# Kernel optimization log

Hardware: AMD Instinct MI355X
Metric: run time of the kernel (lower is better)

The kernel has to match this reference:

```python
import jax, jax.numpy as jnp
import numpy as np

N_PAPER = 100000
N_LABEL = 128
E_CITES = 1600000
E_IS = 100000
F_IN = 128
HID = 128
EMB = 64


def _seg_sum(data, ids, n):
    return jax.ops.segment_sum(data, ids, num_segments=n)


def gcn_conv(x, src, dst, W, b, n):
    # PyG GCNConv: out = D^-1/2 (A+I) D^-1/2 (x W) + b
    h = x @ W
    deg = _seg_sum(jnp.ones(src.shape[0], h.dtype), dst, n) + 1.0  # +1 self loop
    dinv = jax.lax.rsqrt(deg)
    norm = dinv[src] * dinv[dst]                      # [E]
    out = _seg_sum(h[src] * norm[:, None], dst, n)    # neighbor messages
    out = out + (dinv * dinv)[:, None] * h            # self-loop term
    return out + b


def graph_conv(x_src, x_dst, src, dst, W_rel, b_rel, W_root, n_dst):
    # PyG GraphConv: out = lin_rel(sum_j x_j) + lin_root(x_i)
    agg = _seg_sum(x_src[src], dst, n_dst)
    return agg @ W_rel + b_rel + x_dst @ W_root


def hetero_layer(xp, xl, cs, cd, iss, isd, p):
    # outputs onto 'paper' from cites (GCN) and rev_is (GraphConv label->paper): mean of 2
    o_cites = gcn_conv(xp, cs, cd, p['gcn_W'], p['gcn_b'], N_PAPER)
    o_rev = graph_conv(xl, xp, isd, iss, p['rev_relW'], p['rev_relb'], p['rev_rootW'], N_PAPER)
    o_paper = 0.5 * (o_cites + o_rev)
    # output onto 'label' from is (GraphConv paper->label): single conv, mean is identity
    o_label = graph_conv(xp, xl, iss, isd, p['is_relW'], p['is_relb'], p['is_rootW'], N_LABEL)
    return o_paper, o_label


def _init_params(key, d_in, d_out, pfx):
    ks = jax.random.split(key, 8)
    s = 1.0 / np.sqrt(d_in)
    return {
        'gcn_W': jax.random.normal(ks[0], (d_in, d_out), jnp.float32) * s,
        'gcn_b': jnp.zeros((d_out,), jnp.float32),
        'is_relW': jax.random.normal(ks[1], (d_in, d_out), jnp.float32) * s,
        'is_relb': jnp.zeros((d_out,), jnp.float32),
        'is_rootW': jax.random.normal(ks[2], (d_in, d_out), jnp.float32) * s,
        'rev_relW': jax.random.normal(ks[3], (d_in, d_out), jnp.float32) * s,
        'rev_relb': jnp.zeros((d_out,), jnp.float32),
        'rev_rootW': jax.random.normal(ks[4], (d_in, d_out), jnp.float32) * s,
    }


def setup_inputs() -> dict:
    key = jax.random.key(0)
    ks = jax.random.split(key, 10)
    inp = {
        'x_paper': jax.random.normal(ks[0], (N_PAPER, F_IN), jnp.float32),
        'x_label': jax.random.normal(ks[1], (N_LABEL, F_IN), jnp.float32),
        'cites_src': jax.random.randint(ks[2], (E_CITES,), 0, N_PAPER, jnp.int32),
        'cites_dst': jax.random.randint(ks[3], (E_CITES,), 0, N_PAPER, jnp.int32),
        'is_src': jax.random.randint(ks[4], (E_IS,), 0, N_PAPER, jnp.int32),
        'is_dst': jax.random.randint(ks[5], (E_IS,), 0, N_LABEL, jnp.int32),
    }
    p1 = _init_params(ks[6], F_IN, HID, 'l1')
    p2 = _init_params(ks[7], HID, EMB, 'l2')
    for k, v in p1.items():
        inp['l1_' + k] = v
    for k, v in p2.items():
        inp['l2_' + k] = v
    return inp


def reference(x_paper, x_label, cites_src, cites_dst, is_src, is_dst,
              l1_gcn_W, l1_gcn_b, l1_is_relW, l1_is_relb, l1_is_rootW,
              l1_rev_relW, l1_rev_relb, l1_rev_rootW,
              l2_gcn_W, l2_gcn_b, l2_is_relW, l2_is_relb, l2_is_rootW,
              l2_rev_relW, l2_rev_relb, l2_rev_rootW):
    p1 = dict(gcn_W=l1_gcn_W, gcn_b=l1_gcn_b, is_relW=l1_is_relW, is_relb=l1_is_relb,
              is_rootW=l1_is_rootW, rev_relW=l1_rev_relW, rev_relb=l1_rev_relb, rev_rootW=l1_rev_rootW)
    p2 = dict(gcn_W=l2_gcn_W, gcn_b=l2_gcn_b, is_relW=l2_is_relW, is_relb=l2_is_relb,
              is_rootW=l2_is_rootW, rev_relW=l2_rev_relW, rev_relb=l2_rev_relb, rev_rootW=l2_rev_rootW)
    hp, hl = hetero_layer(x_paper, x_label, cites_src, cites_dst, is_src, is_dst, p1)
    hp, hl = jax.nn.relu(hp), jax.nn.relu(hl)
    zp, zl = hetero_layer(hp, hl, cites_src, cites_dst, is_src, is_dst, p2)
    return zp, zl
```

## Files before the change

### kernel.cpp

```cpp
#include <hip/hip_runtime.h>
#include <hip/hip_bf16.h>

#define N_PAPER 100000
#define N_LABEL 128
#define E_CITES 1600000
#define E_IS    100000
#define NBKT    98
#define A2_CHUNK 2048
#define LSPLIT  8
#define CAPC    24576
#define CAPR    2048
#define CAPL    8192

typedef __bf16 bf16x8 __attribute__((ext_vector_type(8)));
typedef float  f32x4  __attribute__((ext_vector_type(4)));
typedef float  f32x2  __attribute__((ext_vector_type(2)));

static __device__ __forceinline__ float bf_lo(unsigned u) {
    union { unsigned u; float f; } v; v.u = u << 16; return v.f;
}
static __device__ __forceinline__ float bf_hi(unsigned u) {
    union { unsigned u; float f; } v; v.u = u & 0xffff0000u; return v.f;
}
static __device__ __forceinline__ unsigned pk_bf(float a, float b) {
    __hip_bfloat16 x = __float2bfloat16(a), y = __float2bfloat16(b);
    unsigned short ux = *(unsigned short*)&x, uy = *(unsigned short*)&y;
    return (unsigned)ux | ((unsigned)uy << 16);
}
static __device__ __forceinline__ unsigned char enc_fp8(float v) {
    return (unsigned char)(__builtin_amdgcn_cvt_pk_fp8_f32(v, v, 0, false) & 0xFF);
}
static __device__ __forceinline__ void dec4(unsigned u, float* o) {
    f32x2 a = __builtin_amdgcn_cvt_pk_f32_fp8((int)u, false);
    f32x2 b = __builtin_amdgcn_cvt_pk_f32_fp8((int)u, true);
    o[0] = a[0]; o[1] = a[1]; o[2] = b[0]; o[3] = b[1];
}

#define NSC ((E_CITES + A2_CHUNK - 1) / A2_CHUNK)
#define NSI ((E_IS + A2_CHUNK - 1) / A2_CHUNK)
__global__ __launch_bounds__(256) void fused_scatter(
    const int* __restrict__ cd, const int* __restrict__ cs,
    const int* __restrict__ iss, const int* __restrict__ isd,
    int* __restrict__ bcur_c, unsigned* __restrict__ ebuf_c,
    int* __restrict__ bcur_r, unsigned* __restrict__ ebuf_r,
    int* __restrict__ bcur_l, unsigned* __restrict__ ebuf_l)
{
    __shared__ int sk[A2_CHUNK], sv[A2_CHUNK];
    __shared__ int h[128], base[128], cur[128];
    int b = blockIdx.x, t = threadIdx.x;
    const int* key; const int* val; int E, shift, b0, cap; int* bcur; unsigned* ebuf;
    if (b < NSC)            { key = cd;  val = cs;  E = E_CITES; bcur = bcur_c; ebuf = ebuf_c; shift = 10; cap = CAPC; b0 = b; }
    else if (b < NSC + NSI) { key = iss; val = isd; E = E_IS;    bcur = bcur_r; ebuf = ebuf_r; shift = 10; cap = CAPR; b0 = b - NSC; }
    else                    { key = isd; val = iss; E = E_IS;    bcur = bcur_l; ebuf = ebuf_l; shift = 0;  cap = CAPL; b0 = b - NSC - NSI; }
    int e0 = b0 * A2_CHUNK;
    int n = min(A2_CHUNK, E - e0);
    for (int i = t; i < 128; i += 256) h[i] = 0;
    __syncthreads();
    for (int i = t; i < n; i += 256) {
        int k = key[e0 + i], v = val[e0 + i];
        sk[i] = k; sv[i] = v;
        atomicAdd(&h[k >> shift], 1);
    }
    __syncthreads();
    for (int i = t; i < 128; i += 256) { base[i] = atomicAdd(&bcur[i], h[i]); cur[i] = 0; }
    __syncthreads();
    for (int i = t; i < n; i += 256) {
        int bb = sk[i] >> shift;
        int p = base[bb] + atomicAdd(&cur[bb], 1);
        ebuf[(size_t)bb * cap + p] = ((unsigned)(sk[i] & 1023) << 17) | (unsigned)sv[i];
    }
}

__global__ __launch_bounds__(1024) void fused_csr(
    const unsigned* __restrict__ ebuf_c, const int* __restrict__ bcnt_c,
    int2* __restrict__ rp2_c, int* __restrict__ col_c, float* __restrict__ dinv,
    const unsigned* __restrict__ ebuf_r, const int* __restrict__ bcnt_r,
    int2* __restrict__ rp2_r, int* __restrict__ col_r)
{
    __shared__ int hist[1024];
    __shared__ int sc[1024];
    int bb = blockIdx.x, t = threadIdx.x;
    const unsigned* ebuf; const int* bcnt; int2* rp2; int* col; float* dv; int b, cap;
    if (bb < NBKT) { ebuf = ebuf_c; bcnt = bcnt_c; rp2 = rp2_c; col = col_c; dv = dinv; b = bb; cap = CAPC; }
    else           { ebuf = ebuf_r; bcnt = bcnt_r; rp2 = rp2_r; col = col_r; dv = nullptr; b = bb - NBKT; cap = CAPR; }
    size_t s = (size_t)b * cap;
    int n = bcnt[b];
    hist[t] = 0;
    __syncthreads();
    for (int i = t; i < n; i += 1024)
        atomicAdd(&hist[ebuf[s + i] >> 17], 1);
    __syncthreads();
    int v = hist[t];
    sc[t] = v;
    __syncthreads();
    for (int off = 1; off < 1024; off <<= 1) {
        int u = (t >= off) ? sc[t - off] : 0;
        __syncthreads();
        sc[t] += u;
        __syncthreads();
    }
    int excl = sc[t] - v;
    int node = b * 1024 + t;
    if (node < N_PAPER) {
        rp2[node] = make_int2((int)(s + excl), (int)(s + excl + v));
        if (dv) dv[node] = rsqrtf((float)v + 1.0f);
    }
    __syncthreads();
    hist[t] = (int)(s + excl);
    __syncthreads();
    for (int i = t; i < n; i += 1024) {
        unsigned u = ebuf[s + i];
        int p = atomicAdd(&hist[u >> 17], 1);
        col[p] = (int)(u & 0x1FFFFu);
    }
}

__global__ __launch_bounds__(256) void fused_prep(
    const float* __restrict__ g1, const float* __restrict__ r1, __hip_bfloat16* __restrict__ Wp1,
    const float* __restrict__ g2, const float* __restrict__ r2, __hip_bfloat16* __restrict__ Wp2,
    const float* __restrict__ xl, const float* __restrict__ W1rev, float* __restrict__ yrev1)
{
    int b = blockIdx.x, t = threadIdx.x;
    if (b < 128 + 64) {
        bool big = (b < 128);
        const float* g = big ? g1 : g2;
        const float* r = big ? r1 : r2;
        __hip_bfloat16* Wp = big ? Wp1 : Wp2;
        int DG = big ? 128 : 64;
        int i = (big ? b : (b - 128)) * 256 + t;
        int j    = i & 7;
        int lane = (i >> 3) & 63;
        int ks   = (i >> 9) & 3;
        int nt   = i >> 11;
        int k = ks * 32 + (lane >> 4) * 8 + j;
        int c = nt * 16 + (lane & 15);
        float v = (c < DG) ? g[k * DG + c] : r[k * DG + (c - DG)];
        Wp[i] = __float2bfloat16(v);
        return;
    }
    __shared__ float xrow[2][128];
    int bb = b - (128 + 64);
    int half = t >> 7, tt = t & 127;
    int l = bb * 2 + half;
    xrow[half][tt] = xl[(size_t)l * 128 + tt];
    __syncthreads();
    float o = 0.f;
    for (int k = 0; k < 128; ++k) o = fmaf(xrow[half][k], W1rev[k * 128 + tt], o);
    yrev1[(size_t)l * 128 + tt] = o;
}

template<int DG, bool AF32>
__global__ __launch_bounds__(512) void gemm_mfma(
    const void* __restrict__ Av, const __hip_bfloat16* __restrict__ Wp,
    const float* __restrict__ dinv,
    unsigned char* __restrict__ Hg, __hip_bfloat16* __restrict__ Hr, int M)
{
    constexpr int NT2 = 2 * DG / 16;
    __shared__ __hip_bfloat16 wlds[NT2 * 2048];
    int tid = threadIdx.x;
    for (int i = tid; i < NT2 * 256; i += 512)
        *(bf16x8*)(wlds + (size_t)i * 8) = *(const bf16x8*)(Wp + (size_t)i * 8);
    __syncthreads();

    int wv = tid >> 6, lane = tid & 63;
    int m0 = blockIdx.x * 128 + wv * 16;
    int row = m0 + (lane & 15);
    int rowc = min(row, M - 1);
    int kg = lane >> 4;

    bf16x8 a[4];
    if constexpr (AF32) {
        const float* ap = (const float*)Av + (size_t)rowc * 128 + kg * 8;
        #pragma unroll
        for (int ks = 0; ks < 4; ++ks) {
            float4 v0 = *(const float4*)(ap + ks * 32);
            float4 v1 = *(const float4*)(ap + ks * 32 + 4);
            bf16x8 f;
            f[0] = (__bf16)v0.x; f[1] = (__bf16)v0.y; f[2] = (__bf16)v0.z; f[3] = (__bf16)v0.w;
            f[4] = (__bf16)v1.x; f[5] = (__bf16)v1.y; f[6] = (__bf16)v1.z; f[7] = (__bf16)v1.w;
            a[ks] = f;
        }
    } else {
        const __hip_bfloat16* ap = (const __hip_bfloat16*)Av + (size_t)rowc * 128 + kg * 8;
        #pragma unroll
        for (int ks = 0; ks < 4; ++ks)
            a[ks] = *(const bf16x8*)(ap + ks * 32);
    }

    f32x4 acc[NT2] = {};
    #pragma unroll
    for (int ks = 0; ks < 4; ++ks) {
        #pragma unroll
        for (int nt = 0; nt < NT2; ++nt) {
            bf16x8 b = *(const bf16x8*)(wlds + ((size_t)(nt * 4 + ks) * 64 + lane) * 8);
            acc[nt] = __builtin_amdgcn_mfma_f32_16x16x32_bf16(a[ks], b, acc[nt], 0, 0, 0);
        }
    }

    int rbase = m0 + (lane >> 4) * 4;
    int c = lane & 15;
    float ds[4];
    #pragma unroll
    for (int r = 0; r < 4; ++r) {
        int rr = rbase + r;
        ds[r] = (rr < M) ? dinv[rr] : 1.f;
    }
    #pragma unroll
    for (int nt = 0; nt < NT2; ++nt) {
        bool isG = (nt < DG / 16);
        if (isG) {
            int cc = nt * 16 + c;
            #pragma unroll
            for (int r = 0; r < 4; ++r) {
                int rr = rbase + r;
                if (rr < M) Hg[(size_t)rr * DG + cc] = enc_fp8(acc[nt][r] * ds[r]);
            }
        } else {
            int cc = (nt - DG / 16) * 16 + c;
            #pragma unroll
            for (int r = 0; r < 4; ++r) {
                int rr = rbase + r;
                if (rr < M) Hr[(size_t)rr * DG + cc] = __float2bfloat16(acc[nt][r]);
            }
        }
    }
}

template<int D, bool RELU, typename OutT>
__global__ __launch_bounds__(256) void paper_assemble(
    const unsigned char* __restrict__ Hg, const __hip_bfloat16* __restrict__ Hr,
    const int2* __restrict__ rp2_c, const int* __restrict__ col_c,
    const float* __restrict__ dinv,
    const int2* __restrict__ rp2_r, const int* __restrict__ col_r,
    const float* __restrict__ yrev,
    const float* __restrict__ gcn_b, const float* __restrict__ rev_relb,
    OutT* __restrict__ out)
{
    constexpr int GL = (D == 128) ? 16 : 8;
    constexpr int NGRP = 64 / GL;
    int w = (int)((blockIdx.x * 256 + threadIdx.x) >> 6);
    if (w >= N_PAPER) return;
    int lane = threadIdx.x & 63;
    int grp = lane / GL, sub = lane % GL;
    unsigned d0 = (unsigned)sub * 8;
    f32x2 a2[4] = {};
    int2 se = rp2_c[w];
    int e = se.y;
    int j = se.x + grp;
    for (; j + NGRP < e; j += 2 * NGRP) {
        unsigned o0 = (unsigned)col_c[j] * D + d0;
        unsigned o1 = (unsigned)col_c[j + NGRP] * D + d0;
        uint2 u = *(const uint2*)(Hg + o0);
        uint2 v = *(const uint2*)(Hg + o1);
        a2[0] += __builtin_amdgcn_cvt_pk_f32_fp8((int)u.x, false);
        a2[1] += __builtin_amdgcn_cvt_pk_f32_fp8((int)u.x, true);
        a2[2] += __builtin_amdgcn_cvt_pk_f32_fp8((int)u.y, false);
        a2[3] += __builtin_amdgcn_cvt_pk_f32_fp8((int)u.y, true);
        a2[0] += __builtin_amdgcn_cvt_pk_f32_fp8((int)v.x, false);
        a2[1] += __builtin_amdgcn_cvt_pk_f32_fp8((int)v.x, true);
        a2[2] += __builtin_amdgcn_cvt_pk_f32_fp8((int)v.y, false);
        a2[3] += __builtin_amdgcn_cvt_pk_f32_fp8((int)v.y, true);
    }
    if (j < e) {
        unsigned o0 = (unsigned)col_c[j] * D + d0;
        uint2 u = *(const uint2*)(Hg + o0);
        a2[0] += __builtin_amdgcn_cvt_pk_f32_fp8((int)u.x, false);
        a2[1] += __builtin_amdgcn_cvt_pk_f32_fp8((int)u.x, true);
        a2[2] += __builtin_amdgcn_cvt_pk_f32_fp8((int)u.y, false);
        a2[3] += __builtin_amdgcn_cvt_pk_f32_fp8((int)u.y, true);
    }
    float acc[8];
    #pragma unroll
    for (int k = 0; k < 8; ++k) acc[k] = a2[k >> 1][k & 1];
    #pragma unroll
    for (int k = 0; k < 8; ++k) {
        #pragma unroll
        for (int off = GL; off < 64; off <<= 1)
            acc[k] += __shfl_xor(acc[k], off);
    }
    if (grp != 0) return;

    float di = dinv[w];
    float res[8], sg[8], sr[8];
    const unsigned char* hg = Hg + ((unsigned)w * D + d0);
    const __hip_bfloat16* hr = Hr + (size_t)w * D + d0;
    uint2 ug = *(const uint2*)hg;
    dec4(ug.x, sg); dec4(ug.y, sg + 4);
    uint4 ur = *(const uint4*)hr;
    sr[0] = bf_lo(ur.x); sr[1] = bf_hi(ur.x); sr[2] = bf_lo(ur.y); sr[3] = bf_hi(ur.y);
    sr[4] = bf_lo(ur.z); sr[5] = bf_hi(ur.z); sr[6] = bf_lo(ur.w); sr[7] = bf_hi(ur.w);
    #pragma unroll
    for (int k = 0; k < 8; ++k)
        res[k] = di * (acc[k] + sg[k]) + sr[k] + gcn_b[d0 + k] + rev_relb[d0 + k];

    int2 se2 = rp2_r[w];
    for (int jj = se2.x; jj < se2.y; ++jj) {
        const float* yr = yrev + (size_t)col_r[jj] * D + d0;
        #pragma unroll
        for (int k = 0; k < 8; ++k) res[k] += yr[k];
    }
    #pragma unroll
    for (int k = 0; k < 8; ++k) {
        res[k] *= 0.5f;
        if (RELU) res[k] = fmaxf(res[k], 0.f);
    }
    if constexpr (sizeof(OutT) == 2) {
        uint4 o = make_uint4(pk_bf(res[0], res[1]), pk_bf(res[2], res[3]),
                             pk_bf(res[4], res[5]), pk_bf(res[6], res[7]));
        *(uint4*)(out + (size_t)w * D + d0) = o;
    } else {
        *(float4*)((float*)out + (size_t)w * D + d0) =
            make_float4(res[0], res[1], res[2], res[3]);
        *(float4*)((float*)out + (size_t)w * D + d0 + 4) =
            make_float4(res[4], res[5], res[6], res[7]);
    }
}

template<bool AF32>
__global__ __launch_bounds__(128) void label_agg(
    const void* __restrict__ Xv,
    const int* __restrict__ cnt_l, const unsigned* __restrict__ ebuf_l,
    float* __restrict__ partialL)
{
    int l = blockIdx.x, sp = blockIdx.y, t = threadIdx.x;
    int n = cnt_l[l];
    size_t s = (size_t)l * CAPL;
    int per = (n + LSPLIT - 1) / LSPLIT;
    int b = sp * per;
    int en = min(b + per, n);
    float acc = 0.f;
    for (int m = b; m < en; ++m) {
        size_t idx = (size_t)(ebuf_l[s + m] & 0x1FFFFu) * 128 + t;
        if constexpr (AF32) acc += ((const float*)Xv)[idx];
        else                acc += __bfloat162float(((const __hip_bfloat16*)Xv)[idx]);
    }
    partialL[((size_t)l * LSPLIT + sp) * 128 + t] = acc;
}

template<int DOUT, bool RELU, bool YREV2>
__global__ __launch_bounds__(128) void label_finish(
    const float* __restrict__ partialL, const float* __restrict__ Xdst,
    const float* __restrict__ relW, const float* __restrict__ rootW,
    const float* __restrict__ relb, float* __restrict__ out,
    const float* __restrict__ W2rev, float* __restrict__ yrev2)
{
    __shared__ float arow[128];
    __shared__ float xrow[128];
    __shared__ float hrow[128];
    int l = blockIdx.x, t = threadIdx.x;
    float a = 0.f;
    #pragma unroll
    for (int sp = 0; sp < LSPLIT; ++sp)
        a += partialL[((size_t)l * LSPLIT + sp) * 128 + t];
    arow[t] = a;
    xrow[t] = Xdst[(size_t)l * 128 + t];
    __syncthreads();
    float o = 0.f;
    if (t < DOUT) {
        o = relb[t];
        for (int k = 0; k < 128; ++k)
            o = fmaf(arow[k], relW[k * DOUT + t], fmaf(xrow[k], rootW[k * DOUT + t], o));
        if (RELU) o = fmaxf(o, 0.f);
        out[(size_t)l * DOUT + t] = o;
    }
    if constexpr (YREV2) {
        hrow[t] = o;
        __syncthreads();
        if (t < 64) {
            float y = 0.f;
            for (int k = 0; k < 128; ++k)
                y = fmaf(hrow[k], W2rev[k * 64 + t], y);
            yrev2[(size_t)l * 64 + t] = y;
        }
    }
}

extern "C" void kernel_launch(void* const* d_in, const int* in_sizes, int n_in,
                              void* d_out, int out_size, void* d_ws, size_t ws_size,
                              hipStream_t stream)
{
    const float* xp          = (const float*)d_in[0];
    const float* xl          = (const float*)d_in[1];
    const int*   cs          = (const int*)d_in[2];
    const int*   cd          = (const int*)d_in[3];
    const int*   iss         = (const int*)d_in[4];
    const int*   isd         = (const int*)d_in[5];
    const float* l1_gcn_W    = (const float*)d_in[6];
    const float* l1_gcn_b    = (const float*)d_in[7];
    const float* l1_is_relW  = (const float*)d_in[8];
    const float* l1_is_relb  = (const float*)d_in[9];
    const float* l1_is_rootW = (const float*)d_in[10];
    const float* l1_rev_relW = (const float*)d_in[11];
    const float* l1_rev_relb = (const float*)d_in[12];
    const float* l1_rev_rootW= (const float*)d_in[13];
    const float* l2_gcn_W    = (const float*)d_in[14];
    const float* l2_gcn_b    = (const float*)d_in[15];
    const float* l2_is_relW  = (const float*)d_in[16];
    const float* l2_is_relb  = (const float*)d_in[17];
    const float* l2_is_rootW = (const float*)d_in[18];
    const float* l2_rev_relW = (const float*)d_in[19];
    const float* l2_rev_relb = (const float*)d_in[20];
    const float* l2_rev_rootW= (const float*)d_in[21];

    char* ws = (char*)d_ws;
    size_t off = 0;
    auto alloc = [&](size_t bytes) {
        char* p = ws + off;
        off += (bytes + 255) & ~(size_t)255;
        return p;
    };
    __hip_bfloat16* hp1   = (__hip_bfloat16*)alloc((size_t)N_PAPER * 128 * 2);
    unsigned char*  Hg    = (unsigned char*)alloc((size_t)N_PAPER * 128);
    __hip_bfloat16* Hr    = (__hip_bfloat16*)alloc((size_t)N_PAPER * 128 * 2);
    unsigned* ebuf_c = (unsigned*)alloc((size_t)NBKT * CAPC * 4);
    int*      col_c  = (int*)alloc((size_t)NBKT * CAPC * 4);
    unsigned* ebuf_r = (unsigned*)alloc((size_t)NBKT * CAPR * 4);
    int*      col_r  = (int*)alloc((size_t)NBKT * CAPR * 4);
    unsigned* ebuf_l = (unsigned*)alloc((size_t)N_LABEL * CAPL * 4);
    int2*  rp2_c = (int2*)alloc((size_t)N_PAPER * 8);
    int2*  rp2_r = (int2*)alloc((size_t)N_PAPER * 8);
    int*   bcur_c = (int*)alloc((size_t)(NBKT + NBKT + 128) * 4);
    int*   bcur_r = bcur_c + NBKT;
    int*   bcur_l = bcur_r + NBKT;
    float* dinv  = (float*)alloc((size_t)N_PAPER * 4);
    __hip_bfloat16* Wp1 = (__hip_bfloat16*)alloc((size_t)32768 * 2);
    __hip_bfloat16* Wp2 = (__hip_bfloat16*)alloc((size_t)16384 * 2);
    float* yrev1 = (float*)alloc(128 * 128 * 4);
    float* yrev2 = (float*)alloc(128 * 64 * 4);
    float* hl1   = (float*)alloc(128 * 128 * 4);
    float* partialL = (float*)alloc((size_t)N_LABEL * LSPLIT * 128 * 4);

    float* zp = (float*)d_out;
    float* zl = (float*)d_out + (size_t)N_PAPER * 64;

    hipMemsetAsync(bcur_c, 0, (size_t)(NBKT + NBKT + 128) * 4, stream);

    fused_scatter<<<NSC + 2 * NSI, 256, 0, stream>>>(cd, cs, iss, isd,
                                                     bcur_c, ebuf_c, bcur_r, ebuf_r, bcur_l, ebuf_l);
    fused_csr<<<2 * NBKT, 1024, 0, stream>>>(ebuf_c, bcur_c, rp2_c, col_c, dinv,
                                             ebuf_r, bcur_r, rp2_r, col_r);
    fused_prep<<<128 + 64 + 64, 256, 0, stream>>>(
        l1_gcn_W, l1_rev_rootW, Wp1, l2_gcn_W, l2_rev_rootW, Wp2,
        xl, l1_rev_relW, yrev1);

    gemm_mfma<128, true><<<(N_PAPER + 127) / 128, 512, 0, stream>>>(xp, Wp1, dinv, Hg, Hr, N_PAPER);
    paper_assemble<128, true, __hip_bfloat16><<<(N_PAPER + 3) / 4, 256, 0, stream>>>(
        Hg, Hr, rp2_c, col_c, dinv, rp2_r, col_r, yrev1, l1_gcn_b, l1_rev_relb, hp1);
    label_agg<true><<<dim3(N_LABEL, LSPLIT), 128, 0, stream>>>(xp, bcur_l, ebuf_l, partialL);
    label_finish<128, true, true><<<N_LABEL, 128, 0, stream>>>(
        partialL, xl, l1_is_relW, l1_is_rootW, l1_is_relb, hl1, l2_rev_relW, yrev2);

    gemm_mfma<64, false><<<(N_PAPER + 127) / 128, 512, 0, stream>>>(hp1, Wp2, dinv, Hg, Hr, N_PAPER);
    paper_assemble<64, false, float><<<(N_PAPER + 3) / 4, 256, 0, stream>>>(
        Hg, Hr, rp2_c, col_c, dinv, rp2_r, col_r, yrev2, l2_gcn_b, l2_rev_relb, zp);
    label_agg<false><<<dim3(N_LABEL, LSPLIT), 128, 0, stream>>>(hp1, bcur_l, ebuf_l, partialL);
    label_finish<64, false, false><<<N_LABEL, 128, 0, stream>>>(
        partialL, hl1, l2_is_relW, l2_is_rootW, l2_is_relb, zl, nullptr, nullptr);
}
```

Baseline: 307.0 us.

## Slice fp8 GCN feature table into column slabs for cache-local gathers

The GEMM now writes the fp8 scaled features as column slices: eight 16-column slabs for layer 1 and eight 8-column slabs for layer 2, each stored contiguously across all nodes. The assemble kernels are rewritten so that each block handles one slice for a group of nodes, with lanes spreading neighbours over 8 slots. The aim is to keep each slice's gather working set (about 1.6 MB or 0.8 MB) resident in L2/LLC instead of gathering from the full table. The cost is that the CSR edge list and column indices are re-read once per slice, and each gather is only 8 bytes per lane.

```diff
diff --git a/kernel.cpp b/kernel.cpp
--- a/kernel.cpp
+++ b/kernel.cpp
@@ -11,6 +11,8 @@
 #define CAPC    24576
 #define CAPR    2048
 #define CAPL    8192
+#define NS1     ((size_t)N_PAPER * 16)
+#define NS2     ((size_t)N_PAPER * 8)
 
 typedef __bf16 bf16x8 __attribute__((ext_vector_type(8)));
 typedef float  f32x4  __attribute__((ext_vector_type(4)));
@@ -209,11 +211,17 @@
     for (int nt = 0; nt < NT2; ++nt) {
         bool isG = (nt < DG / 16);
         if (isG) {
-            int cc = nt * 16 + c;
             #pragma unroll
             for (int r = 0; r < 4; ++r) {
                 int rr = rbase + r;
-                if (rr < M) Hg[(size_t)rr * DG + cc] = enc_fp8(acc[nt][r] * ds[r]);
+                if (rr < M) {
+                    unsigned char q = enc_fp8(acc[nt][r] * ds[r]);
+                    if constexpr (DG == 128) {
+                        Hg[(size_t)nt * NS1 + (size_t)rr * 16 + c] = q;
+                    } else {
+                        Hg[(size_t)(nt * 2 + (c >> 3)) * NS2 + (size_t)rr * 8 + (c & 7)] = q;
+                    }
+                }
             }
         } else {
             int cc = (nt - DG / 16) * 16 + c;
@@ -226,44 +234,95 @@
     }
 }
 
-template<int D, bool RELU, typename OutT>
-__global__ __launch_bounds__(256) void paper_assemble(
+__global__ __launch_bounds__(256) void paper_assemble1(
     const unsigned char* __restrict__ Hg, const __hip_bfloat16* __restrict__ Hr,
     const int2* __restrict__ rp2_c, const int* __restrict__ col_c,
     const float* __restrict__ dinv,
     const int2* __restrict__ rp2_r, const int* __restrict__ col_r,
     const float* __restrict__ yrev,
     const float* __restrict__ gcn_b, const float* __restrict__ rev_relb,
-    OutT* __restrict__ out)
-{
-    constexpr int GL = (D == 128) ? 16 : 8;
-    constexpr int NGRP = 64 / GL;
-    int w = (int)((blockIdx.x * 256 + threadIdx.x) >> 6);
-    if (w >= N_PAPER) return;
-    int lane = threadIdx.x & 63;
-    int grp = lane / GL, sub = lane % GL;
-    unsigned d0 = (unsigned)sub * 8;
+    __hip_bfloat16* __restrict__ out)
+{
+    int b = blockIdx.x;
+    int slice = b & 7;
+    int nb = (b >> 3) * 16;
+    int wv = threadIdx.x >> 6, lane = threadIdx.x & 63;
+    int n = nb + wv * 4 + (lane >> 4);
+    int slot = (lane >> 1) & 7;
+    int sub = lane & 1;
+    const unsigned char* tbl = Hg + (size_t)slice * NS1;
+
     f32x2 a2[4] = {};
-    int2 se = rp2_c[w];
-    int e = se.y;
-    int j = se.x + grp;
-    for (; j + NGRP < e; j += 2 * NGRP) {
-        unsigned o0 = (unsigned)col_c[j] * D + d0;
-        unsigned o1 = (unsigned)col_c[j + NGRP] * D + d0;
-        uint2 u = *(const uint2*)(Hg + o0);
-        uint2 v = *(const uint2*)(Hg + o1);
+    int2 se = rp2_c[n];
+    for (int j = se.x + slot; j < se.y; j += 8) {
+        unsigned col = (unsigned)col_c[j];
+        uint2 u = *(const uint2*)(tbl + col * 16 + sub * 8);
         a2[0] += __builtin_amdgcn_cvt_pk_f32_fp8((int)u.x, false);
         a2[1] += __builtin_amdgcn_cvt_pk_f32_fp8((int)u.x, true);
         a2[2] += __builtin_amdgcn_cvt_pk_f32_fp8((int)u.y, false);
         a2[3] += __builtin_amdgcn_cvt_pk_f32_fp8((int)u.y, true);
-        a2[0] += __builtin_amdgcn_cvt_pk_f32_fp8((int)v.x, false);
-        a2[1] += __builtin_amdgcn_cvt_pk_f32_fp8((int)v.x, true);
-        a2[2] += __builtin_amdgcn_cvt_pk_f32_fp8((int)v.y, false);
-        a2[3] += __builtin_amdgcn_cvt_pk_f32_fp8((int)v.y, true);
-    }
-    if (j < e) {
-        unsigned o0 = (unsigned)col_c[j] * D + d0;
-        uint2 u = *(const uint2*)(Hg + o0);
+    }
+    float acc[8];
+    #pragma unroll
+    for (int k = 0; k < 8; ++k) acc[k] = a2[k >> 1][k & 1];
+    #pragma unroll
+    for (int k = 0; k < 8; ++k) {
+        acc[k] += __shfl_xor(acc[k], 2);
+        acc[k] += __shfl_xor(acc[k], 4);
+        acc[k] += __shfl_xor(acc[k], 8);
+    }
+    if (slot != 0) return;
+
+    unsigned d0 = (unsigned)slice * 16 + (unsigned)sub * 8;
+    float di = dinv[n];
+    float sg[8], sr[8], res[8];
+    uint2 ug = *(const uint2*)(tbl + (unsigned)n * 16 + sub * 8);
+    dec4(ug.x, sg); dec4(ug.y, sg + 4);
+    uint4 ur = *(const uint4*)(Hr + (size_t)n * 128 + d0);
+    sr[0] = bf_lo(ur.x); sr[1] = bf_hi(ur.x); sr[2] = bf_lo(ur.y); sr[3] = bf_hi(ur.y);
+    sr[4] = bf_lo(ur.z); sr[5] = bf_hi(ur.z); sr[6] = bf_lo(ur.w); sr[7] = bf_hi(ur.w);
+    #pragma unroll
+    for (int k = 0; k < 8; ++k)
+        res[k] = di * (acc[k] + sg[k]) + sr[k] + gcn_b[d0 + k] + rev_relb[d0 + k];
+
+    int2 se2 = rp2_r[n];
+    for (int jj = se2.x; jj < se2.y; ++jj) {
+        const float* yr = yrev + (size_t)col_r[jj] * 128 + d0;
+        #pragma unroll
+        for (int k = 0; k < 8; ++k) res[k] += yr[k];
+    }
+    #pragma unroll
+    for (int k = 0; k < 8; ++k) {
+        res[k] *= 0.5f;
+        res[k] = fmaxf(res[k], 0.f);
+    }
+    uint4 o = make_uint4(pk_bf(res[0], res[1]), pk_bf(res[2], res[3]),
+                         pk_bf(res[4], res[5]), pk_bf(res[6], res[7]));
+    *(uint4*)(out + (size_t)n * 128 + d0) = o;
+}
+
+__global__ __launch_bounds__(256) void paper_assemble2(
+    const unsigned char* __restrict__ Hg, const __hip_bfloat16* __restrict__ Hr,
+    const int2* __restrict__ rp2_c, const int* __restrict__ col_c,
+    const float* __restrict__ dinv,
+    const int2* __restrict__ rp2_r, const int* __restrict__ col_r,
+    const float* __restrict__ yrev,
+    const float* __restrict__ gcn_b, const float* __restrict__ rev_relb,
+    float* __restrict__ out)
+{
+    int b = blockIdx.x;
+    int slice = b & 7;
+    int nb = (b >> 3) * 32;
+    int wv = threadIdx.x >> 6, lane = threadIdx.x & 63;
+    int n = nb + wv * 8 + (lane >> 3);
+    int slot = lane & 7;
+    const unsigned char* tbl = Hg + (size_t)slice * NS2;
+
+    f32x2 a2[4] = {};
+    int2 se = rp2_c[n];
+    for (int j = se.x + slot; j < se.y; j += 8) {
+        unsigned col = (unsigned)col_c[j];
+        uint2 u = *(const uint2*)(tbl + col * 8);
         a2[0] += __builtin_amdgcn_cvt_pk_f32_fp8((int)u.x, false);
         a2[1] += __builtin_amdgcn_cvt_pk_f32_fp8((int)u.x, true);
         a2[2] += __builtin_amdgcn_cvt_pk_f32_fp8((int)u.y, false);
@@ -274,46 +333,36 @@
     for (int k = 0; k < 8; ++k) acc[k] = a2[k >> 1][k & 1];
     #pragma unroll
     for (int k = 0; k < 8; ++k) {
-        #pragma unroll
-        for (int off = GL; off < 64; off <<= 1)
-            acc[k] += __shfl_xor(acc[k], off);
-    }
-    if (grp != 0) return;
-
-    float di = dinv[w];
-    float res[8], sg[8], sr[8];
-    const unsigned char* hg = Hg + ((unsigned)w * D + d0);
-    const __hip_bfloat16* hr = Hr + (size_t)w * D + d0;
-    uint2 ug = *(const uint2*)hg;
+        acc[k] += __shfl_xor(acc[k], 1);
+        acc[k] += __shfl_xor(acc[k], 2);
+        acc[k] += __shfl_xor(acc[k], 4);
+    }
+    if (slot != 0) return;
+
+    unsigned d0 = (unsigned)slice * 8;
+    float di = dinv[n];
+    float sg[8], sr[8], res[8];
+    uint2 ug = *(const uint2*)(tbl + (unsigned)n * 8);
     dec4(ug.x, sg); dec4(ug.y, sg + 4);
-    uint4 ur = *(const uint4*)hr;
+    uint4 ur = *(const uint4*)(Hr + (size_t)n * 64 + d0);
     sr[0] = bf_lo(ur.x); sr[1] = bf_hi(ur.x); sr[2] = bf_lo(ur.y); sr[3] = bf_hi(ur.y);
     sr[4] = bf_lo(ur.z); sr[5] = bf_hi(ur.z); sr[6] = bf_lo(ur.w); sr[7] = bf_hi(ur.w);
     #pragma unroll
     for (int k = 0; k < 8; ++k)
         res[k] = di * (acc[k] + sg[k]) + sr[k] + gcn_b[d0 + k] + rev_relb[d0 + k];
 
-    int2 se2 = rp2_r[w];
+    int2 se2 = rp2_r[n];
     for (int jj = se2.x; jj < se2.y; ++jj) {
-        const float* yr = yrev + (size_t)col_r[jj] * D + d0;
+        const float* yr = yrev + (size_t)col_r[jj] * 64 + d0;
         #pragma unroll
         for (int k = 0; k < 8; ++k) res[k] += yr[k];
     }
     #pragma unroll
-    for (int k = 0; k < 8; ++k) {
-        res[k] *= 0.5f;
-        if (RELU) res[k] = fmaxf(res[k], 0.f);
-    }
-    if constexpr (sizeof(OutT) == 2) {
-        uint4 o = make_uint4(pk_bf(res[0], res[1]), pk_bf(res[2], res[3]),
-                             pk_bf(res[4], res[5]), pk_bf(res[6], res[7]));
-        *(uint4*)(out + (size_t)w * D + d0) = o;
-    } else {
-        *(float4*)((float*)out + (size_t)w * D + d0) =
-            make_float4(res[0], res[1], res[2], res[3]);
-        *(float4*)((float*)out + (size_t)w * D + d0 + 4) =
-            make_float4(res[4], res[5], res[6], res[7]);
-    }
+    for (int k = 0; k < 8; ++k) res[k] *= 0.5f;
+    *(float4*)(out + (size_t)n * 64 + d0) =
+        make_float4(res[0], res[1], res[2], res[3]);
+    *(float4*)(out + (size_t)n * 64 + d0 + 4) =
+        make_float4(res[4], res[5], res[6], res[7]);
 }
 
 template<bool AF32>
@@ -444,14 +493,14 @@
         xl, l1_rev_relW, yrev1);
 
     gemm_mfma<128, true><<<(N_PAPER + 127) / 128, 512, 0, stream>>>(xp, Wp1, dinv, Hg, Hr, N_PAPER);
-    paper_assemble<128, true, __hip_bfloat16><<<(N_PAPER + 3) / 4, 256, 0, stream>>>(
+    paper_assemble1<<<8 * (N_PAPER / 16), 256, 0, stream>>>(
         Hg, Hr, rp2_c, col_c, dinv, rp2_r, col_r, yrev1, l1_gcn_b, l1_rev_relb, hp1);
     label_agg<true><<<dim3(N_LABEL, LSPLIT), 128, 0, stream>>>(xp, bcur_l, ebuf_l, partialL);
     label_finish<128, true, true><<<N_LABEL, 128, 0, stream>>>(
         partialL, xl, l1_is_relW, l1_is_rootW, l1_is_relb, hl1, l2_rev_relW, yrev2);
 
     gemm_mfma<64, false><<<(N_PAPER + 127) / 128, 512, 0, stream>>>(hp1, Wp2, dinv, Hg, Hr, N_PAPER);
-    paper_assemble<64, false, float><<<(N_PAPER + 3) / 4, 256, 0, stream>>>(
+    paper_assemble2<<<8 * (N_PAPER / 32), 256, 0, stream>>>(
         Hg, Hr, rp2_c, col_c, dinv, rp2_r, col_r, yrev2, l2_gcn_b, l2_rev_relb, zp);
     label_agg<false><<<dim3(N_LABEL, LSPLIT), 128, 0, stream>>>(hp1, bcur_l, ebuf_l, partialL);
     label_finish<64, false, false><<<N_LABEL, 128, 0, stream>>>(
```

Result: slower. 408.6 us (+33.1%).
